# Kernel optimization log

Hardware: AMD Instinct MI355X
Metric: run time of the kernel (lower is better)

The kernel has to match this reference:

```python
import jax, jax.numpy as jnp
import numpy as np

L = 4        # num decoder layers
H = 8        # heads
D = 512      # d_model
DFF = 2048   # ffn hidden
V = 8000     # target vocab
B = 16       # batch
S_ENC = 128  # encoder seq len
T = 32       # decode target_length
START, END, NULL = 1, 2, 0
NEG = -1e9
EPS = 1e-6


def sinusoid_pos(max_len, d):
    pos = np.arange(max_len)[:, None].astype(np.float32)
    i = np.arange(d)[None, :].astype(np.float32)
    ang = pos / np.power(10000.0, (2.0 * np.floor(i / 2.0)) / d)
    pe = np.where(np.arange(d)[None, :] % 2 == 0, np.sin(ang), np.cos(ang))
    return jnp.asarray(pe[None], jnp.float32)  # [1, max_len, d]


def setup_inputs() -> dict:
    key = jax.random.key(0)
    ks = jax.random.split(key, 16)
    g = lambda k, shape: jax.random.normal(k, shape, jnp.float32) * 0.02
    return {
        "target_length": T,
        "encoder_output": jax.random.normal(ks[0], (B, S_ENC, D), jnp.float32),
        "padding_mask": jnp.zeros((B, S_ENC), jnp.float32),  # 1.0 where padded
        "embed": g(ks[1], (V, D)),
        "wq": g(ks[2], (L, D, D)), "wk": g(ks[3], (L, D, D)),
        "wv": g(ks[4], (L, D, D)), "wo": g(ks[5], (L, D, D)),
        "cwq": g(ks[6], (L, D, D)), "cwk": g(ks[7], (L, D, D)),
        "cwv": g(ks[8], (L, D, D)), "cwo": g(ks[9], (L, D, D)),
        "w1": g(ks[10], (L, D, DFF)), "b1": jnp.zeros((L, DFF), jnp.float32),
        "w2": g(ks[11], (L, DFF, D)), "b2": jnp.zeros((L, D), jnp.float32),
        "ln_g": jnp.ones((L, 3, D), jnp.float32), "ln_b": jnp.zeros((L, 3, D), jnp.float32),
        "fc_w": g(ks[12], (D, V)), "fc_b": jnp.zeros((V,), jnp.float32),
    }


def ln(x, g, b):
    m = jnp.mean(x, axis=-1, keepdims=True)
    v = jnp.mean(jnp.square(x - m), axis=-1, keepdims=True)
    return (x - m) * jax.lax.rsqrt(v + EPS) * g + b


def mha(q_in, kv_in, wq, wk, wv, wo, mask):
    Bn, Sq, d = q_in.shape
    dh = d // H
    q = (q_in @ wq).reshape(Bn, Sq, H, dh)
    k = (kv_in @ wk).reshape(Bn, -1, H, dh)
    v = (kv_in @ wv).reshape(Bn, -1, H, dh)
    s = jnp.einsum('bqhd,bkhd->bhqk', q, k) / jnp.sqrt(jnp.float32(dh)) + mask
    a = jax.nn.softmax(s, axis=-1)
    o = jnp.einsum('bhqk,bkhd->bqhd', a, v).reshape(Bn, Sq, d)
    return o @ wo


def decoder_stack(x, encoder_output, self_mask, cross_mask,
                  wq, wk, wv, wo, cwq, cwk, cwv, cwo,
                  w1, b1, w2, b2, ln_g, ln_b):
    for i in range(L):
        a = mha(x, x, wq[i], wk[i], wv[i], wo[i], self_mask)
        x = ln(x + a, ln_g[i, 0], ln_b[i, 0])
        a2 = mha(x, encoder_output, cwq[i], cwk[i], cwv[i], cwo[i], cross_mask)
        x = ln(x + a2, ln_g[i, 1], ln_b[i, 1])
        f = jax.nn.relu(x @ w1[i] + b1[i]) @ w2[i] + b2[i]
        x = ln(x + f, ln_g[i, 2], ln_b[i, 2])
    return x


def reference(target_length, encoder_output, padding_mask, embed,
              wq, wk, wv, wo, cwq, cwk, cwv, cwo,
              w1, b1, w2, b2, ln_g, ln_b, fc_w, fc_b):
    Bn, S, d = encoder_output.shape
    Tp1 = target_length + 1
    pos_enc = sinusoid_pos(Tp1, d)
    sqrt_d = jnp.sqrt(jnp.float32(d))
    cross_mask = padding_mask[:, None, None, :] * NEG  # [B,1,1,S_enc]
    tokens0 = jnp.full((Bn, Tp1), NULL, jnp.int32).at[:, 0].set(START)
    done0 = jnp.zeros((Bn,), bool)

    def step(carry, t):
        tokens, done = carry
        # re-embed the whole (fixed-size, masked) prefix buffer each step
        x = embed[tokens] * sqrt_d + pos_enc
        # only positions <= t are valid keys; no look-ahead mask (matches original)
        self_mask = jnp.where(jnp.arange(Tp1) <= t, 0.0, NEG)[None, None, None, :]
        x = decoder_stack(x, encoder_output, self_mask, cross_mask,
                          wq, wk, wv, wo, cwq, cwk, cwv, cwo,
                          w1, b1, w2, b2, ln_g, ln_b)
        out = x[:, t, :] @ fc_w + fc_b  # logits at last valid position
        max_idx = jnp.argmax(out, axis=-1).astype(jnp.int32)
        done = done | (max_idx == END)
        tok = jnp.where(done, jnp.int32(NULL), max_idx)
        tokens = tokens.at[:, t + 1].set(tok)
        return (tokens, done), None

    (tokens, done), _ = jax.lax.scan(step, (tokens0, done0), jnp.arange(target_length))
    return tokens[:, 1:].astype(jnp.int64)
```

## Files before the change

kernel.cpp:

```cpp
#include <hip/hip_runtime.h>
#include <math.h>

#define L_   4
#define H_   8
#define D_   512
#define DH   64
#define DFF_ 2048
#define V_   8000
#define B_   16
#define SENC 128
#define T_   32
#define TP1  33
#define NEGV -1e9f
#define EPSV 1e-6f
#define SQRTD 22.627416997969522f
#define XSZ  ((size_t)TP1 * B_ * D_)

__global__ __launch_bounds__(128) void gemm32_k(
    const float* __restrict__ A, const float* __restrict__ W,
    const float* __restrict__ bias, float* __restrict__ C,
    int M, int N, int K, int kchunk, size_t pstride, int relu, int tmode)
{
    __shared__ __align__(16) float As[16][32];
    __shared__ __align__(16) float Bs[16][64];
    int tid = threadIdx.x;
    int tx = tid & 15, ty = tid >> 4;
    int m0 = blockIdx.y * 32, n0 = blockIdx.x * 64;
    int kbeg = blockIdx.z * kchunk, kend = kbeg + kchunk;
    C += (size_t)blockIdx.z * pstride;
    int am = tid >> 2, aseg = tid & 3;
    int bk = tid >> 4, bc4 = (tid & 15) * 4;
    float acc[4][4] = {};
    for (int k0 = kbeg; k0 < kend; k0 += 16) {
        int gm = m0 + am;
        float4 av = make_float4(0.f, 0.f, 0.f, 0.f);
        if (gm < M) av = *(const float4*)&A[(size_t)gm * K + k0 + aseg * 4];
        As[aseg * 4 + 0][am] = av.x;
        As[aseg * 4 + 1][am] = av.y;
        As[aseg * 4 + 2][am] = av.z;
        As[aseg * 4 + 3][am] = av.w;
        *(float4*)&Bs[bk][bc4] =
            *(const float4*)&W[(size_t)(k0 + bk) * N + n0 + bc4];
        *(float4*)&Bs[bk + 8][bc4] =
            *(const float4*)&W[(size_t)(k0 + bk + 8) * N + n0 + bc4];
        __syncthreads();
        #pragma unroll
        for (int kk = 0; kk < 16; kk++) {
            float4 a4 = *(const float4*)&As[kk][ty * 4];
            float4 b4 = *(const float4*)&Bs[kk][tx * 4];
            float a[4] = {a4.x, a4.y, a4.z, a4.w};
            float b[4] = {b4.x, b4.y, b4.z, b4.w};
            #pragma unroll
            for (int i = 0; i < 4; i++)
                #pragma unroll
                for (int j = 0; j < 4; j++)
                    acc[i][j] += a[i] * b[j];
        }
        __syncthreads();
    }
    #pragma unroll
    for (int i = 0; i < 4; i++) {
        int gm = m0 + ty * 4 + i;
        if (gm >= M) continue;
        #pragma unroll
        for (int j = 0; j < 4; j++) {
            int gn = n0 + tx * 4 + j;
            float v = acc[i][j];
            if (bias) v += bias[gn];
            if (relu) v = fmaxf(v, 0.f);
            if (tmode == 1)
                C[(size_t)(gm >> 7) * 65536 + (size_t)gn * SENC + (gm & 127)] = v;
            else
                C[(size_t)gm * N + gn] = v;
        }
    }
}

__global__ __launch_bounds__(128) void gemm_qkv_k(
    const float* __restrict__ A, const float* __restrict__ W0,
    const float* __restrict__ W1, const float* __restrict__ W2,
    float* __restrict__ Cb, int M)
{
    __shared__ __align__(16) float As[16][32];
    __shared__ __align__(16) float Bs[16][64];
    int sel = blockIdx.x >> 3;
    const float* W = (sel == 0) ? W0 : ((sel == 1) ? W1 : W2);
    float* C = Cb + (size_t)sel * XSZ;
    int tid = threadIdx.x;
    int tx = tid & 15, ty = tid >> 4;
    int m0 = blockIdx.y * 32, n0 = (blockIdx.x & 7) * 64;
    int am = tid >> 2, aseg = tid & 3;
    int bk = tid >> 4, bc4 = (tid & 15) * 4;
    float acc[4][4] = {};
    for (int k0 = 0; k0 < D_; k0 += 16) {
        int gm = m0 + am;
        float4 av = make_float4(0.f, 0.f, 0.f, 0.f);
        if (gm < M) av = *(const float4*)&A[(size_t)gm * D_ + k0 + aseg * 4];
        As[aseg * 4 + 0][am] = av.x;
        As[aseg * 4 + 1][am] = av.y;
        As[aseg * 4 + 2][am] = av.z;
        As[aseg * 4 + 3][am] = av.w;
        *(float4*)&Bs[bk][bc4] =
            *(const float4*)&W[(size_t)(k0 + bk) * D_ + n0 + bc4];
        *(float4*)&Bs[bk + 8][bc4] =
            *(const float4*)&W[(size_t)(k0 + bk + 8) * D_ + n0 + bc4];
        __syncthreads();
        #pragma unroll
        for (int kk = 0; kk < 16; kk++) {
            float4 a4 = *(const float4*)&As[kk][ty * 4];
            float4 b4 = *(const float4*)&Bs[kk][tx * 4];
            float a[4] = {a4.x, a4.y, a4.z, a4.w};
            float b[4] = {b4.x, b4.y, b4.z, b4.w};
            #pragma unroll
            for (int i = 0; i < 4; i++)
                #pragma unroll
                for (int j = 0; j < 4; j++)
                    acc[i][j] += a[i] * b[j];
        }
        __syncthreads();
    }
    #pragma unroll
    for (int i = 0; i < 4; i++) {
        int gm = m0 + ty * 4 + i;
        if (gm >= M) continue;
        #pragma unroll
        for (int j = 0; j < 4; j++) {
            int gn = n0 + tx * 4 + j;
            if (sel == 1)
                C[(size_t)(gm & 15) * 16896 + (size_t)gn * TP1 + (gm >> 4)] =
                    acc[i][j];
            else
                C[(size_t)gm * D_ + gn] = acc[i][j];
        }
    }
}

__global__ void init_k(int* __restrict__ tokens, int* __restrict__ done,
                       float* __restrict__ cmask, const float* __restrict__ pm)
{
    int tid = threadIdx.x + blockIdx.x * 256;
    if (tid < B_ * TP1) tokens[tid] = ((tid % TP1) == 0) ? 1 : 0;
    if (tid < B_) done[tid] = 0;
    if (tid < B_ * SENC) cmask[tid] = pm[tid] * NEGV;
}

__global__ __launch_bounds__(256) void embed_k(
    const float* __restrict__ embed, const int* __restrict__ tokens,
    float* __restrict__ x)
{
    int p = blockIdx.x;
    int b = blockIdx.y;
    int tok = tokens[b * TP1 + p];
    const float* e = embed + (size_t)tok * D_;
    float* xr = x + ((size_t)p * B_ + b) * D_;
    for (int d = threadIdx.x; d < D_; d += 256) {
        float fd = (float)(2 * (d / 2)) / (float)D_;
        float ang = (float)p / powf(10000.f, fd);
        float pe = (d & 1) ? cosf(ang) : sinf(ang);
        xr[d] = e[d] * SQRTD + pe;
    }
}

__device__ __forceinline__ float block_sum(float s) {
    __shared__ float red[4];
    #pragma unroll
    for (int off = 32; off; off >>= 1) s += __shfl_xor(s, off);
    if ((threadIdx.x & 63) == 0) red[threadIdx.x >> 6] = s;
    __syncthreads();
    float tot = red[0] + red[1] + red[2] + red[3];
    __syncthreads();
    return tot;
}

__global__ __launch_bounds__(256) void self_fused_k(
    const float* __restrict__ q, const float* __restrict__ kT,
    const float* __restrict__ v, const float* __restrict__ wo,
    float* __restrict__ x, const float* __restrict__ gam,
    const float* __restrict__ bet, int P)
{
    int r = blockIdx.x;
    int b = r & 15;
    int tid = threadIdx.x;
    __shared__ float qrow[D_], attnrow[D_];
    __shared__ float scs[H_][32];
    __shared__ float inv[H_];
    qrow[tid]       = q[(size_t)r * D_ + tid];
    qrow[tid + 256] = q[(size_t)r * D_ + tid + 256];
    __syncthreads();
    {
        int kp = tid & 31, h = tid >> 5;
        float acc = 0.f;
        if (kp < P) {
            const float* kb = kT + ((size_t)(b * 8 + h) * 64) * TP1 + kp;
            for (int d = 0; d < 64; d++)
                acc += qrow[h * 64 + d] * kb[(size_t)d * TP1];
        }
        scs[h][kp] = acc * 0.125f;
    }
    __syncthreads();
    if (tid < 8) {
        float mx = -1e30f;
        for (int j = 0; j < P; j++) mx = fmaxf(mx, scs[tid][j]);
        float sum = 0.f;
        for (int j = 0; j < P; j++) {
            float e = expf(scs[tid][j] - mx);
            scs[tid][j] = e;
            sum += e;
        }
        inv[tid] = 1.f / sum;
    }
    __syncthreads();
    {
        int h0 = tid >> 6, h1 = h0 + 4;
        float o0 = 0.f, o1 = 0.f;
        for (int j = 0; j < P; j++) {
            const float* vr = v + ((size_t)j * B_ + b) * D_;
            o0 += scs[h0][j] * vr[tid];
            o1 += scs[h1][j] * vr[tid + 256];
        }
        attnrow[tid]       = o0 * inv[h0];
        attnrow[tid + 256] = o1 * inv[h1];
    }
    __syncthreads();
    float v0 = x[(size_t)r * D_ + tid];
    float v1 = x[(size_t)r * D_ + tid + 256];
    for (int k0 = 0; k0 < D_; k0++) {
        float a = attnrow[k0];
        v0 += a * wo[(size_t)k0 * D_ + tid];
        v1 += a * wo[(size_t)k0 * D_ + tid + 256];
    }
    float mean = block_sum(v0 + v1) * (1.f / 512.f);
    float d0 = v0 - mean, d1 = v1 - mean;
    float var = block_sum(d0 * d0 + d1 * d1) * (1.f / 512.f);
    float rs = rsqrtf(var + EPSV);
    x[(size_t)r * D_ + tid]       = d0 * rs * gam[tid] + bet[tid];
    x[(size_t)r * D_ + tid + 256] = d1 * rs * gam[tid + 256] + bet[tid + 256];
}

__global__ __launch_bounds__(256) void cross_fused_k(
    const float* __restrict__ KcT, const float* __restrict__ Vc,
    const float* __restrict__ cmask, const float* __restrict__ cwq,
    const float* __restrict__ cwo, float* __restrict__ x,
    const float* __restrict__ gam, const float* __restrict__ bet)
{
    int r = blockIdx.x;
    int b = r & 15;
    int tid = threadIdx.x;
    __shared__ float xs[D_], qrow[D_], attnrow[D_];
    __shared__ float scs[H_][SENC];
    __shared__ float inv[H_];
    xs[tid]       = x[(size_t)r * D_ + tid];
    xs[tid + 256] = x[(size_t)r * D_ + tid + 256];
    __syncthreads();
    {
        float q0 = 0.f, q1 = 0.f;
        for (int k0 = 0; k0 < D_; k0++) {
            float a = xs[k0];
            q0 += a * cwq[(size_t)k0 * D_ + tid];
            q1 += a * cwq[(size_t)k0 * D_ + tid + 256];
        }
        qrow[tid] = q0;
        qrow[tid + 256] = q1;
    }
    __syncthreads();
    #pragma unroll
    for (int j = 0; j < 4; j++) {
        int idx = tid + j * 256;
        int h = idx >> 7, s = idx & 127;
        const float* kb = KcT + ((size_t)(b * 512 + h * 64)) * SENC + s;
        float acc = 0.f;
        for (int d = 0; d < 64; d++)
            acc += qrow[h * 64 + d] * kb[(size_t)d * SENC];
        scs[h][s] = acc * 0.125f + cmask[b * SENC + s];
    }
    __syncthreads();
    if (tid < 8) {
        float mx = -1e30f;
        for (int s = 0; s < SENC; s++) mx = fmaxf(mx, scs[tid][s]);
        float sum = 0.f;
        for (int s = 0; s < SENC; s++) {
            float e = expf(scs[tid][s] - mx);
            scs[tid][s] = e;
            sum += e;
        }
        inv[tid] = 1.f / sum;
    }
    __syncthreads();
    {
        int h0 = tid >> 6, h1 = h0 + 4;
        float o0 = 0.f, o1 = 0.f;
        for (int s = 0; s < SENC; s++) {
            const float* vr = Vc + ((size_t)b * SENC + s) * D_;
            o0 += scs[h0][s] * vr[tid];
            o1 += scs[h1][s] * vr[tid + 256];
        }
        attnrow[tid]       = o0 * inv[h0];
        attnrow[tid + 256] = o1 * inv[h1];
    }
    __syncthreads();
    float v0 = xs[tid];
    float v1 = xs[tid + 256];
    for (int k0 = 0; k0 < D_; k0++) {
        float a = attnrow[k0];
        v0 += a * cwo[(size_t)k0 * D_ + tid];
        v1 += a * cwo[(size_t)k0 * D_ + tid + 256];
    }
    float mean = block_sum(v0 + v1) * (1.f / 512.f);
    float d0 = v0 - mean, d1 = v1 - mean;
    float var = block_sum(d0 * d0 + d1 * d1) * (1.f / 512.f);
    float rs = rsqrtf(var + EPSV);
    x[(size_t)r * D_ + tid]       = d0 * rs * gam[tid] + bet[tid];
    x[(size_t)r * D_ + tid + 256] = d1 * rs * gam[tid + 256] + bet[tid + 256];
}

__global__ __launch_bounds__(256) void ln_red_k(
    float* __restrict__ x, const float* __restrict__ parts, size_t pstride,
    int nparts, const float* __restrict__ bias,
    const float* __restrict__ gam, const float* __restrict__ bet)
{
    int r = blockIdx.x;
    float* xr = x + (size_t)r * D_;
    int tid = threadIdx.x;
    float v0 = xr[tid];
    float v1 = xr[tid + 256];
    for (int s = 0; s < nparts; s++) {
        const float* pr = parts + (size_t)s * pstride + (size_t)r * D_;
        v0 += pr[tid];
        v1 += pr[tid + 256];
    }
    if (bias) { v0 += bias[tid]; v1 += bias[tid + 256]; }
    float mean = block_sum(v0 + v1) * (1.f / 512.f);
    float d0 = v0 - mean, d1 = v1 - mean;
    float var = block_sum(d0 * d0 + d1 * d1) * (1.f / 512.f);
    float rs = rsqrtf(var + EPSV);
    xr[tid]       = d0 * rs * gam[tid] + bet[tid];
    xr[tid + 256] = d1 * rs * gam[tid + 256] + bet[tid + 256];
}

__global__ __launch_bounds__(256) void logits_k(
    const float* __restrict__ x, const float* __restrict__ fcw,
    const float* __restrict__ fcb, float* __restrict__ logits, int t)
{
    __shared__ float xs[B_][D_];
    __shared__ float red[4][64][B_];
    int tid = threadIdx.x;
    for (int i = tid; i < B_ * D_; i += 256) {
        int b = i >> 9, d = i & 511;
        xs[b][d] = x[((size_t)t * B_ + b) * D_ + d];
    }
    __syncthreads();
    int lane = tid & 63, ks = tid >> 6;
    int col = blockIdx.x * 64 + lane;
    float acc[B_] = {};
    int kb = ks * 128;
    for (int k = kb; k < kb + 128; k++) {
        float w = fcw[(size_t)k * V_ + col];
        #pragma unroll
        for (int b = 0; b < B_; b++) acc[b] += xs[b][k] * w;
    }
    #pragma unroll
    for (int b = 0; b < B_; b++) red[ks][lane][b] = acc[b];
    __syncthreads();
    if (ks == 0) {
        float bias = fcb[col];
        #pragma unroll
        for (int b = 0; b < B_; b++) {
            float s = red[0][lane][b] + red[1][lane][b]
                    + red[2][lane][b] + red[3][lane][b];
            logits[(size_t)b * V_ + col] = s + bias;
        }
    }
}

__global__ __launch_bounds__(256) void argmax_k(
    const float* __restrict__ logits, int* __restrict__ tokens,
    int* __restrict__ done, int t)
{
    int b = blockIdx.x;
    const float* lr = logits + (size_t)b * V_;
    float bv = -1e30f; int bi = 0x7fffffff;
    for (int v = threadIdx.x; v < V_; v += 256) {
        float val = lr[v];
        if (val > bv) { bv = val; bi = v; }
    }
    __shared__ float sv[256];
    __shared__ int si[256];
    sv[threadIdx.x] = bv; si[threadIdx.x] = bi;
    __syncthreads();
    for (int s = 128; s; s >>= 1) {
        if (threadIdx.x < s) {
            float ov = sv[threadIdx.x + s]; int oi = si[threadIdx.x + s];
            if (ov > sv[threadIdx.x] ||
                (ov == sv[threadIdx.x] && oi < si[threadIdx.x])) {
                sv[threadIdx.x] = ov; si[threadIdx.x] = oi;
            }
        }
        __syncthreads();
    }
    if (threadIdx.x == 0) {
        int idx = si[0];
        int dn = done[b] | (idx == 2 ? 1 : 0);
        done[b] = dn;
        tokens[b * TP1 + t + 1] = dn ? 0 : idx;
    }
}

__global__ void writeout_k(const int* __restrict__ tokens, int* __restrict__ out)
{
    int i = threadIdx.x + blockIdx.x * 256;
    if (i < B_ * T_) {
        int b = i / T_, j = i % T_;
        out[i] = tokens[b * TP1 + j + 1];
    }
}

extern "C" void kernel_launch(void* const* d_in, const int* in_sizes, int n_in,
                              void* d_out, int out_size, void* d_ws, size_t ws_size,
                              hipStream_t stream)
{
    const float* enc   = (const float*)d_in[1];
    const float* pm    = (const float*)d_in[2];
    const float* embed = (const float*)d_in[3];
    const float* wq    = (const float*)d_in[4];
    const float* wk    = (const float*)d_in[5];
    const float* wv    = (const float*)d_in[6];
    const float* wo    = (const float*)d_in[7];
    const float* cwq   = (const float*)d_in[8];
    const float* cwk   = (const float*)d_in[9];
    const float* cwv   = (const float*)d_in[10];
    const float* cwo   = (const float*)d_in[11];
    const float* w1    = (const float*)d_in[12];
    const float* b1    = (const float*)d_in[13];
    const float* w2    = (const float*)d_in[14];
    const float* b2    = (const float*)d_in[15];
    const float* ln_g  = (const float*)d_in[16];
    const float* ln_b  = (const float*)d_in[17];
    const float* fcw   = (const float*)d_in[18];
    const float* fcb   = (const float*)d_in[19];

    float* ws = (float*)d_ws;
    size_t off = 0;
    float* x     = ws + off; off += XSZ;
    float* qkv   = ws + off; off += 3 * XSZ;
    float* parts = ws + off; off += 4 * XSZ;
    float* ffnh  = ws + off; off += (size_t)TP1 * B_ * DFF_;
    float* logits= ws + off; off += (size_t)B_ * V_;
    float* KcT   = ws + off; off += (size_t)L_ * B_ * SENC * D_;
    float* Vc    = ws + off; off += (size_t)L_ * B_ * SENC * D_;
    float* cmask = ws + off; off += (size_t)B_ * SENC;
    int* tokens  = (int*)(ws + off); off += (B_ * TP1 + 63) & ~63;
    int* done    = (int*)(ws + off); off += 64;

    init_k<<<8, 256, 0, stream>>>(tokens, done, cmask, pm);

    const size_t KVL = (size_t)B_ * SENC * D_;
    for (int l = 0; l < L_; l++) {
        gemm32_k<<<dim3(8, (B_ * SENC) / 32), 128, 0, stream>>>(
            enc, cwk + (size_t)l * D_ * D_, nullptr, KcT + l * KVL,
            B_ * SENC, D_, D_, D_, 0, 0, 1);
        gemm32_k<<<dim3(8, (B_ * SENC) / 32), 128, 0, stream>>>(
            enc, cwv + (size_t)l * D_ * D_, nullptr, Vc + l * KVL,
            B_ * SENC, D_, D_, D_, 0, 0, 0);
    }

    for (int t = 0; t < T_; t++) {
        int P = t + 1;
        int M = P * B_;
        int mt = (M + 31) / 32;

        embed_k<<<dim3(P, B_), 256, 0, stream>>>(embed, tokens, x);

        for (int l = 0; l < L_; l++) {
            const size_t lw = (size_t)l * D_ * D_;
            gemm_qkv_k<<<dim3(24, mt), 128, 0, stream>>>(
                x, wq + lw, wk + lw, wv + lw, qkv, M);
            self_fused_k<<<M, 256, 0, stream>>>(
                qkv, qkv + XSZ, qkv + 2 * XSZ, wo + lw, x,
                ln_g + (size_t)(l * 3 + 0) * D_, ln_b + (size_t)(l * 3 + 0) * D_, P);
            cross_fused_k<<<M, 256, 0, stream>>>(
                KcT + l * KVL, Vc + l * KVL, cmask, cwq + lw, cwo + lw, x,
                ln_g + (size_t)(l * 3 + 1) * D_, ln_b + (size_t)(l * 3 + 1) * D_);
            gemm32_k<<<dim3(32, mt), 128, 0, stream>>>(
                x, w1 + (size_t)l * D_ * DFF_, b1 + (size_t)l * DFF_, ffnh,
                M, DFF_, D_, D_, 0, 1, 0);
            gemm32_k<<<dim3(8, mt, 4), 128, 0, stream>>>(
                ffnh, w2 + (size_t)l * DFF_ * D_, nullptr, parts,
                M, D_, DFF_, 512, XSZ, 0, 0);
            ln_red_k<<<M, 256, 0, stream>>>(x, parts, XSZ, 4, b2 + (size_t)l * D_,
                ln_g + (size_t)(l * 3 + 2) * D_, ln_b + (size_t)(l * 3 + 2) * D_);
        }

        logits_k<<<V_ / 64, 256, 0, stream>>>(x, fcw, fcb, logits, t);
        argmax_k<<<B_, 256, 0, stream>>>(logits, tokens, done, t);
    }

    writeout_k<<<2, 256, 0, stream>>>(tokens, (int*)d_out);
}
```

Measured before the change: 27.11 ms.

## Double-buffer GEMM tiles, fuse self and cross attention, fold argmax into logits

The GEMM kernels move to 256 threads with 2x4 micro-tiles, padded double-buffered shared tiles and register prefetch of the next k-slice, aiming to overlap loads with compute. The self-attention and cross-attention fused kernels become one kernel per row, removing a launch and a round trip of x through global memory. The logits kernel now does a per-block argmax and writes 125 candidates per batch row, so the final argmax reads candidates instead of full logits. Costs include smaller per-thread work in the GEMM, which may lower ILP, and a longer serial mega kernel per row.

```diff
diff --git a/kernel.cpp b/kernel.cpp
--- a/kernel.cpp
+++ b/kernel.cpp
@@ -16,73 +16,96 @@
 #define SQRTD 22.627416997969522f
 #define XSZ  ((size_t)TP1 * B_ * D_)
 
-__global__ __launch_bounds__(128) void gemm32_k(
+__global__ __launch_bounds__(256) void gemm32_k(
     const float* __restrict__ A, const float* __restrict__ W,
     const float* __restrict__ bias, float* __restrict__ C,
     int M, int N, int K, int kchunk, size_t pstride, int relu, int tmode)
 {
-    __shared__ __align__(16) float As[16][32];
-    __shared__ __align__(16) float Bs[16][64];
+    __shared__ __align__(16) float As[2][16][34];
+    __shared__ __align__(16) float Bs[2][16][68];
     int tid = threadIdx.x;
     int tx = tid & 15, ty = tid >> 4;
     int m0 = blockIdx.y * 32, n0 = blockIdx.x * 64;
-    int kbeg = blockIdx.z * kchunk, kend = kbeg + kchunk;
+    int kbeg = blockIdx.z * kchunk;
+    int niter = kchunk >> 4;
     C += (size_t)blockIdx.z * pstride;
     int am = tid >> 2, aseg = tid & 3;
     int bk = tid >> 4, bc4 = (tid & 15) * 4;
-    float acc[4][4] = {};
-    for (int k0 = kbeg; k0 < kend; k0 += 16) {
-        int gm = m0 + am;
-        float4 av = make_float4(0.f, 0.f, 0.f, 0.f);
-        if (gm < M) av = *(const float4*)&A[(size_t)gm * K + k0 + aseg * 4];
-        As[aseg * 4 + 0][am] = av.x;
-        As[aseg * 4 + 1][am] = av.y;
-        As[aseg * 4 + 2][am] = av.z;
-        As[aseg * 4 + 3][am] = av.w;
-        *(float4*)&Bs[bk][bc4] =
-            *(const float4*)&W[(size_t)(k0 + bk) * N + n0 + bc4];
-        *(float4*)&Bs[bk + 8][bc4] =
-            *(const float4*)&W[(size_t)(k0 + bk + 8) * N + n0 + bc4];
-        __syncthreads();
+    float4 aReg = make_float4(0.f, 0.f, 0.f, 0.f), bReg;
+    {
+        int k0 = kbeg;
+        if (tid < 128) {
+            int gm = m0 + am;
+            if (gm < M) aReg = *(const float4*)&A[(size_t)gm * K + k0 + aseg * 4];
+        }
+        bReg = *(const float4*)&W[(size_t)(k0 + bk) * N + n0 + bc4];
+    }
+    if (tid < 128) {
+        As[0][aseg * 4 + 0][am] = aReg.x;
+        As[0][aseg * 4 + 1][am] = aReg.y;
+        As[0][aseg * 4 + 2][am] = aReg.z;
+        As[0][aseg * 4 + 3][am] = aReg.w;
+    }
+    *(float4*)&Bs[0][bk][bc4] = bReg;
+    __syncthreads();
+    float acc[2][4] = {};
+    for (int it = 0; it < niter; it++) {
+        int cur = it & 1;
+        if (it + 1 < niter) {
+            int k0 = kbeg + (it + 1) * 16;
+            if (tid < 128) {
+                int gm = m0 + am;
+                aReg = make_float4(0.f, 0.f, 0.f, 0.f);
+                if (gm < M) aReg = *(const float4*)&A[(size_t)gm * K + k0 + aseg * 4];
+            }
+            bReg = *(const float4*)&W[(size_t)(k0 + bk) * N + n0 + bc4];
+        }
         #pragma unroll
         for (int kk = 0; kk < 16; kk++) {
-            float4 a4 = *(const float4*)&As[kk][ty * 4];
-            float4 b4 = *(const float4*)&Bs[kk][tx * 4];
-            float a[4] = {a4.x, a4.y, a4.z, a4.w};
-            float b[4] = {b4.x, b4.y, b4.z, b4.w};
-            #pragma unroll
-            for (int i = 0; i < 4; i++)
-                #pragma unroll
-                for (int j = 0; j < 4; j++)
-                    acc[i][j] += a[i] * b[j];
+            float2 a2 = *(const float2*)&As[cur][kk][ty * 2];
+            float4 b4 = *(const float4*)&Bs[cur][kk][tx * 4];
+            acc[0][0] += a2.x * b4.x; acc[0][1] += a2.x * b4.y;
+            acc[0][2] += a2.x * b4.z; acc[0][3] += a2.x * b4.w;
+            acc[1][0] += a2.y * b4.x; acc[1][1] += a2.y * b4.y;
+            acc[1][2] += a2.y * b4.z; acc[1][3] += a2.y * b4.w;
+        }
+        if (it + 1 < niter) {
+            int nxt = 1 - cur;
+            if (tid < 128) {
+                As[nxt][aseg * 4 + 0][am] = aReg.x;
+                As[nxt][aseg * 4 + 1][am] = aReg.y;
+                As[nxt][aseg * 4 + 2][am] = aReg.z;
+                As[nxt][aseg * 4 + 3][am] = aReg.w;
+            }
+            *(float4*)&Bs[nxt][bk][bc4] = bReg;
         }
         __syncthreads();
     }
     #pragma unroll
-    for (int i = 0; i < 4; i++) {
-        int gm = m0 + ty * 4 + i;
+    for (int i = 0; i < 2; i++) {
+        int gm = m0 + ty * 2 + i;
         if (gm >= M) continue;
         #pragma unroll
         for (int j = 0; j < 4; j++) {
             int gn = n0 + tx * 4 + j;
-            float v = acc[i][j];
-            if (bias) v += bias[gn];
-            if (relu) v = fmaxf(v, 0.f);
+            float vv = acc[i][j];
+            if (bias) vv += bias[gn];
+            if (relu) vv = fmaxf(vv, 0.f);
             if (tmode == 1)
-                C[(size_t)(gm >> 7) * 65536 + (size_t)gn * SENC + (gm & 127)] = v;
+                C[(size_t)(gm >> 7) * 65536 + (size_t)gn * SENC + (gm & 127)] = vv;
             else
-                C[(size_t)gm * N + gn] = v;
-        }
-    }
-}
-
-__global__ __launch_bounds__(128) void gemm_qkv_k(
+                C[(size_t)gm * N + gn] = vv;
+        }
+    }
+}
+
+__global__ __launch_bounds__(256) void gemm_qkv_k(
     const float* __restrict__ A, const float* __restrict__ W0,
     const float* __restrict__ W1, const float* __restrict__ W2,
     float* __restrict__ Cb, int M)
 {
-    __shared__ __align__(16) float As[16][32];
-    __shared__ __align__(16) float Bs[16][64];
+    __shared__ __align__(16) float As[2][16][34];
+    __shared__ __align__(16) float Bs[2][16][68];
     int sel = blockIdx.x >> 3;
     const float* W = (sel == 0) ? W0 : ((sel == 1) ? W1 : W2);
     float* C = Cb + (size_t)sel * XSZ;
@@ -91,37 +114,58 @@
     int m0 = blockIdx.y * 32, n0 = (blockIdx.x & 7) * 64;
     int am = tid >> 2, aseg = tid & 3;
     int bk = tid >> 4, bc4 = (tid & 15) * 4;
-    float acc[4][4] = {};
-    for (int k0 = 0; k0 < D_; k0 += 16) {
-        int gm = m0 + am;
-        float4 av = make_float4(0.f, 0.f, 0.f, 0.f);
-        if (gm < M) av = *(const float4*)&A[(size_t)gm * D_ + k0 + aseg * 4];
-        As[aseg * 4 + 0][am] = av.x;
-        As[aseg * 4 + 1][am] = av.y;
-        As[aseg * 4 + 2][am] = av.z;
-        As[aseg * 4 + 3][am] = av.w;
-        *(float4*)&Bs[bk][bc4] =
-            *(const float4*)&W[(size_t)(k0 + bk) * D_ + n0 + bc4];
-        *(float4*)&Bs[bk + 8][bc4] =
-            *(const float4*)&W[(size_t)(k0 + bk + 8) * D_ + n0 + bc4];
-        __syncthreads();
+    float4 aReg = make_float4(0.f, 0.f, 0.f, 0.f), bReg;
+    {
+        if (tid < 128) {
+            int gm = m0 + am;
+            if (gm < M) aReg = *(const float4*)&A[(size_t)gm * D_ + aseg * 4];
+        }
+        bReg = *(const float4*)&W[(size_t)bk * D_ + n0 + bc4];
+    }
+    if (tid < 128) {
+        As[0][aseg * 4 + 0][am] = aReg.x;
+        As[0][aseg * 4 + 1][am] = aReg.y;
+        As[0][aseg * 4 + 2][am] = aReg.z;
+        As[0][aseg * 4 + 3][am] = aReg.w;
+    }
+    *(float4*)&Bs[0][bk][bc4] = bReg;
+    __syncthreads();
+    float acc[2][4] = {};
+    for (int it = 0; it < 32; it++) {
+        int cur = it & 1;
+        if (it + 1 < 32) {
+            int k0 = (it + 1) * 16;
+            if (tid < 128) {
+                int gm = m0 + am;
+                aReg = make_float4(0.f, 0.f, 0.f, 0.f);
+                if (gm < M) aReg = *(const float4*)&A[(size_t)gm * D_ + k0 + aseg * 4];
+            }
+            bReg = *(const float4*)&W[(size_t)(k0 + bk) * D_ + n0 + bc4];
+        }
         #pragma unroll
         for (int kk = 0; kk < 16; kk++) {
-            float4 a4 = *(const float4*)&As[kk][ty * 4];
-            float4 b4 = *(const float4*)&Bs[kk][tx * 4];
-            float a[4] = {a4.x, a4.y, a4.z, a4.w};
-            float b[4] = {b4.x, b4.y, b4.z, b4.w};
-            #pragma unroll
-            for (int i = 0; i < 4; i++)
-                #pragma unroll
-                for (int j = 0; j < 4; j++)
-                    acc[i][j] += a[i] * b[j];
+            float2 a2 = *(const float2*)&As[cur][kk][ty * 2];
+            float4 b4 = *(const float4*)&Bs[cur][kk][tx * 4];
+            acc[0][0] += a2.x * b4.x; acc[0][1] += a2.x * b4.y;
+            acc[0][2] += a2.x * b4.z; acc[0][3] += a2.x * b4.w;
+            acc[1][0] += a2.y * b4.x; acc[1][1] += a2.y * b4.y;
+            acc[1][2] += a2.y * b4.z; acc[1][3] += a2.y * b4.w;
+        }
+        if (it + 1 < 32) {
+            int nxt = 1 - cur;
+            if (tid < 128) {
+                As[nxt][aseg * 4 + 0][am] = aReg.x;
+                As[nxt][aseg * 4 + 1][am] = aReg.y;
+                As[nxt][aseg * 4 + 2][am] = aReg.z;
+                As[nxt][aseg * 4 + 3][am] = aReg.w;
+            }
+            *(float4*)&Bs[nxt][bk][bc4] = bReg;
         }
         __syncthreads();
     }
     #pragma unroll
-    for (int i = 0; i < 4; i++) {
-        int gm = m0 + ty * 4 + i;
+    for (int i = 0; i < 2; i++) {
+        int gm = m0 + ty * 2 + i;
         if (gm >= M) continue;
         #pragma unroll
         for (int j = 0; j < 4; j++) {
@@ -172,28 +216,28 @@
     return tot;
 }
 
-__global__ __launch_bounds__(256) void self_fused_k(
+__global__ __launch_bounds__(256) void attn_mega_k(
     const float* __restrict__ q, const float* __restrict__ kT,
     const float* __restrict__ v, const float* __restrict__ wo,
-    float* __restrict__ x, const float* __restrict__ gam,
-    const float* __restrict__ bet, int P)
-{
-    int r = blockIdx.x;
-    int b = r & 15;
+    const float* __restrict__ KcT, const float* __restrict__ Vc,
+    const float* __restrict__ cmask, const float* __restrict__ cwq,
+    const float* __restrict__ cwo, float* __restrict__ x,
+    const float* __restrict__ lg, const float* __restrict__ lb, int P)
+{
+    int r = blockIdx.x, b = r & 15;
     int tid = threadIdx.x;
-    __shared__ float qrow[D_], attnrow[D_];
-    __shared__ float scs[H_][32];
+    int c0 = tid * 2;
+    __shared__ float xs[D_], arow[D_];
+    __shared__ float scs[H_][SENC];
     __shared__ float inv[H_];
-    qrow[tid]       = q[(size_t)r * D_ + tid];
-    qrow[tid + 256] = q[(size_t)r * D_ + tid + 256];
-    __syncthreads();
     {
         int kp = tid & 31, h = tid >> 5;
         float acc = 0.f;
         if (kp < P) {
+            const float* qr = q + (size_t)r * D_ + h * 64;
             const float* kb = kT + ((size_t)(b * 8 + h) * 64) * TP1 + kp;
-            for (int d = 0; d < 64; d++)
-                acc += qrow[h * 64 + d] * kb[(size_t)d * TP1];
+            #pragma unroll 8
+            for (int d = 0; d < 64; d++) acc += qr[d] * kb[(size_t)d * TP1];
         }
         scs[h][kp] = acc * 0.125f;
     }
@@ -211,56 +255,43 @@
     }
     __syncthreads();
     {
-        int h0 = tid >> 6, h1 = h0 + 4;
+        int h = c0 >> 6;
         float o0 = 0.f, o1 = 0.f;
         for (int j = 0; j < P; j++) {
-            const float* vr = v + ((size_t)j * B_ + b) * D_;
-            o0 += scs[h0][j] * vr[tid];
-            o1 += scs[h1][j] * vr[tid + 256];
-        }
-        attnrow[tid]       = o0 * inv[h0];
-        attnrow[tid + 256] = o1 * inv[h1];
-    }
-    __syncthreads();
-    float v0 = x[(size_t)r * D_ + tid];
-    float v1 = x[(size_t)r * D_ + tid + 256];
-    for (int k0 = 0; k0 < D_; k0++) {
-        float a = attnrow[k0];
-        v0 += a * wo[(size_t)k0 * D_ + tid];
-        v1 += a * wo[(size_t)k0 * D_ + tid + 256];
-    }
-    float mean = block_sum(v0 + v1) * (1.f / 512.f);
-    float d0 = v0 - mean, d1 = v1 - mean;
-    float var = block_sum(d0 * d0 + d1 * d1) * (1.f / 512.f);
-    float rs = rsqrtf(var + EPSV);
-    x[(size_t)r * D_ + tid]       = d0 * rs * gam[tid] + bet[tid];
-    x[(size_t)r * D_ + tid + 256] = d1 * rs * gam[tid + 256] + bet[tid + 256];
-}
-
-__global__ __launch_bounds__(256) void cross_fused_k(
-    const float* __restrict__ KcT, const float* __restrict__ Vc,
-    const float* __restrict__ cmask, const float* __restrict__ cwq,
-    const float* __restrict__ cwo, float* __restrict__ x,
-    const float* __restrict__ gam, const float* __restrict__ bet)
-{
-    int r = blockIdx.x;
-    int b = r & 15;
-    int tid = threadIdx.x;
-    __shared__ float xs[D_], qrow[D_], attnrow[D_];
-    __shared__ float scs[H_][SENC];
-    __shared__ float inv[H_];
-    xs[tid]       = x[(size_t)r * D_ + tid];
-    xs[tid + 256] = x[(size_t)r * D_ + tid + 256];
+            float2 vv = *(const float2*)&v[((size_t)j * B_ + b) * D_ + c0];
+            float w = scs[h][j];
+            o0 += w * vv.x; o1 += w * vv.y;
+        }
+        arow[c0]     = o0 * inv[h];
+        arow[c0 + 1] = o1 * inv[h];
+    }
+    __syncthreads();
+    {
+        float2 xv = *(const float2*)&x[(size_t)r * D_ + c0];
+        float v0 = xv.x, v1 = xv.y;
+        #pragma unroll 8
+        for (int k = 0; k < D_; k++) {
+            float a = arow[k];
+            float2 wv = *(const float2*)&wo[(size_t)k * D_ + c0];
+            v0 += a * wv.x; v1 += a * wv.y;
+        }
+        float mean = block_sum(v0 + v1) * (1.f / 512.f);
+        float d0 = v0 - mean, d1 = v1 - mean;
+        float var = block_sum(d0 * d0 + d1 * d1) * (1.f / 512.f);
+        float rs = rsqrtf(var + EPSV);
+        xs[c0]     = d0 * rs * lg[c0]     + lb[c0];
+        xs[c0 + 1] = d1 * rs * lg[c0 + 1] + lb[c0 + 1];
+    }
     __syncthreads();
     {
         float q0 = 0.f, q1 = 0.f;
-        for (int k0 = 0; k0 < D_; k0++) {
-            float a = xs[k0];
-            q0 += a * cwq[(size_t)k0 * D_ + tid];
-            q1 += a * cwq[(size_t)k0 * D_ + tid + 256];
-        }
-        qrow[tid] = q0;
-        qrow[tid + 256] = q1;
+        #pragma unroll 8
+        for (int k = 0; k < D_; k++) {
+            float a = xs[k];
+            float2 wv = *(const float2*)&cwq[(size_t)k * D_ + c0];
+            q0 += a * wv.x; q1 += a * wv.y;
+        }
+        arow[c0] = q0; arow[c0 + 1] = q1;
     }
     __syncthreads();
     #pragma unroll
@@ -269,8 +300,8 @@
         int h = idx >> 7, s = idx & 127;
         const float* kb = KcT + ((size_t)(b * 512 + h * 64)) * SENC + s;
         float acc = 0.f;
-        for (int d = 0; d < 64; d++)
-            acc += qrow[h * 64 + d] * kb[(size_t)d * SENC];
+        #pragma unroll 8
+        for (int d = 0; d < 64; d++) acc += arow[h * 64 + d] * kb[(size_t)d * SENC];
         scs[h][s] = acc * 0.125f + cmask[b * SENC + s];
     }
     __syncthreads();
@@ -287,30 +318,32 @@
     }
     __syncthreads();
     {
-        int h0 = tid >> 6, h1 = h0 + 4;
+        int h = c0 >> 6;
         float o0 = 0.f, o1 = 0.f;
         for (int s = 0; s < SENC; s++) {
-            const float* vr = Vc + ((size_t)b * SENC + s) * D_;
-            o0 += scs[h0][s] * vr[tid];
-            o1 += scs[h1][s] * vr[tid + 256];
-        }
-        attnrow[tid]       = o0 * inv[h0];
-        attnrow[tid + 256] = o1 * inv[h1];
-    }
-    __syncthreads();
-    float v0 = xs[tid];
-    float v1 = xs[tid + 256];
-    for (int k0 = 0; k0 < D_; k0++) {
-        float a = attnrow[k0];
-        v0 += a * cwo[(size_t)k0 * D_ + tid];
-        v1 += a * cwo[(size_t)k0 * D_ + tid + 256];
-    }
-    float mean = block_sum(v0 + v1) * (1.f / 512.f);
-    float d0 = v0 - mean, d1 = v1 - mean;
-    float var = block_sum(d0 * d0 + d1 * d1) * (1.f / 512.f);
-    float rs = rsqrtf(var + EPSV);
-    x[(size_t)r * D_ + tid]       = d0 * rs * gam[tid] + bet[tid];
-    x[(size_t)r * D_ + tid + 256] = d1 * rs * gam[tid + 256] + bet[tid + 256];
+            float2 vv = *(const float2*)&Vc[((size_t)b * SENC + s) * D_ + c0];
+            float w = scs[h][s];
+            o0 += w * vv.x; o1 += w * vv.y;
+        }
+        arow[c0]     = o0 * inv[h];
+        arow[c0 + 1] = o1 * inv[h];
+    }
+    __syncthreads();
+    {
+        float v0 = xs[c0], v1 = xs[c0 + 1];
+        #pragma unroll 8
+        for (int k = 0; k < D_; k++) {
+            float a = arow[k];
+            float2 wv = *(const float2*)&cwo[(size_t)k * D_ + c0];
+            v0 += a * wv.x; v1 += a * wv.y;
+        }
+        float mean = block_sum(v0 + v1) * (1.f / 512.f);
+        float d0 = v0 - mean, d1 = v1 - mean;
+        float var = block_sum(d0 * d0 + d1 * d1) * (1.f / 512.f);
+        float rs = rsqrtf(var + EPSV);
+        x[(size_t)r * D_ + c0]     = d0 * rs * lg[D_ + c0]     + lb[D_ + c0];
+        x[(size_t)r * D_ + c0 + 1] = d1 * rs * lg[D_ + c0 + 1] + lb[D_ + c0 + 1];
+    }
 }
 
 __global__ __launch_bounds__(256) void ln_red_k(
@@ -339,7 +372,8 @@
 
 __global__ __launch_bounds__(256) void logits_k(
     const float* __restrict__ x, const float* __restrict__ fcw,
-    const float* __restrict__ fcb, float* __restrict__ logits, int t)
+    const float* __restrict__ fcb, float* __restrict__ cand_v,
+    int* __restrict__ cand_i, int t)
 {
     __shared__ float xs[B_][D_];
     __shared__ float red[4][64][B_];
@@ -365,43 +399,49 @@
         float bias = fcb[col];
         #pragma unroll
         for (int b = 0; b < B_; b++) {
-            float s = red[0][lane][b] + red[1][lane][b]
-                    + red[2][lane][b] + red[3][lane][b];
-            logits[(size_t)b * V_ + col] = s + bias;
-        }
-    }
-}
-
-__global__ __launch_bounds__(256) void argmax_k(
-    const float* __restrict__ logits, int* __restrict__ tokens,
-    int* __restrict__ done, int t)
+            float val = red[0][lane][b] + red[1][lane][b]
+                      + red[2][lane][b] + red[3][lane][b] + bias;
+            int idx = col;
+            #pragma unroll
+            for (int off = 32; off; off >>= 1) {
+                float ov = __shfl_down(val, off);
+                int oi = __shfl_down(idx, off);
+                if (ov > val || (ov == val && oi < idx)) { val = ov; idx = oi; }
+            }
+            if (lane == 0) {
+                cand_v[(size_t)b * 125 + blockIdx.x] = val;
+                cand_i[(size_t)b * 125 + blockIdx.x] = idx;
+            }
+        }
+    }
+}
+
+__global__ __launch_bounds__(128) void argmax_k(
+    const float* __restrict__ cand_v, const int* __restrict__ cand_i,
+    int* __restrict__ tokens, int* __restrict__ done, int t)
 {
     int b = blockIdx.x;
-    const float* lr = logits + (size_t)b * V_;
-    float bv = -1e30f; int bi = 0x7fffffff;
-    for (int v = threadIdx.x; v < V_; v += 256) {
-        float val = lr[v];
-        if (val > bv) { bv = val; bi = v; }
-    }
-    __shared__ float sv[256];
-    __shared__ int si[256];
-    sv[threadIdx.x] = bv; si[threadIdx.x] = bi;
-    __syncthreads();
-    for (int s = 128; s; s >>= 1) {
-        if (threadIdx.x < s) {
-            float ov = sv[threadIdx.x + s]; int oi = si[threadIdx.x + s];
-            if (ov > sv[threadIdx.x] ||
-                (ov == sv[threadIdx.x] && oi < si[threadIdx.x])) {
-                sv[threadIdx.x] = ov; si[threadIdx.x] = oi;
+    int tid = threadIdx.x;
+    float val = -1e30f; int idx = 0x7fffffff;
+    if (tid < 125) { val = cand_v[(size_t)b * 125 + tid]; idx = cand_i[(size_t)b * 125 + tid]; }
+    __shared__ float sv[128];
+    __shared__ int si[128];
+    sv[tid] = val; si[tid] = idx;
+    __syncthreads();
+    for (int s = 64; s; s >>= 1) {
+        if (tid < s) {
+            float ov = sv[tid + s]; int oi = si[tid + s];
+            if (ov > sv[tid] || (ov == sv[tid] && oi < si[tid])) {
+                sv[tid] = ov; si[tid] = oi;
             }
         }
         __syncthreads();
     }
-    if (threadIdx.x == 0) {
-        int idx = si[0];
-        int dn = done[b] | (idx == 2 ? 1 : 0);
+    if (tid == 0) {
+        int best = si[0];
+        int dn = done[b] | (best == 2 ? 1 : 0);
         done[b] = dn;
-        tokens[b * TP1 + t + 1] = dn ? 0 : idx;
+        tokens[b * TP1 + t + 1] = dn ? 0 : best;
     }
 }
 
@@ -444,10 +484,11 @@
     float* qkv   = ws + off; off += 3 * XSZ;
     float* parts = ws + off; off += 4 * XSZ;
     float* ffnh  = ws + off; off += (size_t)TP1 * B_ * DFF_;
-    float* logits= ws + off; off += (size_t)B_ * V_;
+    float* cand_v= ws + off; off += (size_t)B_ * 125;
     float* KcT   = ws + off; off += (size_t)L_ * B_ * SENC * D_;
     float* Vc    = ws + off; off += (size_t)L_ * B_ * SENC * D_;
     float* cmask = ws + off; off += (size_t)B_ * SENC;
+    int* cand_i  = (int*)(ws + off); off += (size_t)B_ * 125;
     int* tokens  = (int*)(ws + off); off += (B_ * TP1 + 63) & ~63;
     int* done    = (int*)(ws + off); off += 64;
 
@@ -455,10 +496,10 @@
 
     const size_t KVL = (size_t)B_ * SENC * D_;
     for (int l = 0; l < L_; l++) {
-        gemm32_k<<<dim3(8, (B_ * SENC) / 32), 128, 0, stream>>>(
+        gemm32_k<<<dim3(8, (B_ * SENC) / 32), 256, 0, stream>>>(
             enc, cwk + (size_t)l * D_ * D_, nullptr, KcT + l * KVL,
             B_ * SENC, D_, D_, D_, 0, 0, 1);
-        gemm32_k<<<dim3(8, (B_ * SENC) / 32), 128, 0, stream>>>(
+        gemm32_k<<<dim3(8, (B_ * SENC) / 32), 256, 0, stream>>>(
             enc, cwv + (size_t)l * D_ * D_, nullptr, Vc + l * KVL,
             B_ * SENC, D_, D_, D_, 0, 0, 0);
     }
@@ -472,26 +513,24 @@
 
         for (int l = 0; l < L_; l++) {
             const size_t lw = (size_t)l * D_ * D_;
-            gemm_qkv_k<<<dim3(24, mt), 128, 0, stream>>>(
+            gemm_qkv_k<<<dim3(24, mt), 256, 0, stream>>>(
                 x, wq + lw, wk + lw, wv + lw, qkv, M);
-            self_fused_k<<<M, 256, 0, stream>>>(
-                qkv, qkv + XSZ, qkv + 2 * XSZ, wo + lw, x,
+            attn_mega_k<<<M, 256, 0, stream>>>(
+                qkv, qkv + XSZ, qkv + 2 * XSZ, wo + lw,
+                KcT + l * KVL, Vc + l * KVL, cmask, cwq + lw, cwo + lw, x,
                 ln_g + (size_t)(l * 3 + 0) * D_, ln_b + (size_t)(l * 3 + 0) * D_, P);
-            cross_fused_k<<<M, 256, 0, stream>>>(
-                KcT + l * KVL, Vc + l * KVL, cmask, cwq + lw, cwo + lw, x,
-                ln_g + (size_t)(l * 3 + 1) * D_, ln_b + (size_t)(l * 3 + 1) * D_);
-            gemm32_k<<<dim3(32, mt), 128, 0, stream>>>(
+            gemm32_k<<<dim3(32, mt), 256, 0, stream>>>(
                 x, w1 + (size_t)l * D_ * DFF_, b1 + (size_t)l * DFF_, ffnh,
                 M, DFF_, D_, D_, 0, 1, 0);
-            gemm32_k<<<dim3(8, mt, 4), 128, 0, stream>>>(
+            gemm32_k<<<dim3(8, mt, 4), 256, 0, stream>>>(
                 ffnh, w2 + (size_t)l * DFF_ * D_, nullptr, parts,
                 M, D_, DFF_, 512, XSZ, 0, 0);
             ln_red_k<<<M, 256, 0, stream>>>(x, parts, XSZ, 4, b2 + (size_t)l * D_,
                 ln_g + (size_t)(l * 3 + 2) * D_, ln_b + (size_t)(l * 3 + 2) * D_);
         }
 
-        logits_k<<<V_ / 64, 256, 0, stream>>>(x, fcw, fcb, logits, t);
-        argmax_k<<<B_, 256, 0, stream>>>(logits, tokens, done, t);
+        logits_k<<<V_ / 64, 256, 0, stream>>>(x, fcw, fcb, cand_v, cand_i, t);
+        argmax_k<<<B_, 128, 0, stream>>>(cand_v, cand_i, tokens, done, t);
     }
 
     writeout_k<<<2, 256, 0, stream>>>(tokens, (int*)d_out);
```

Result: faster. 24.32 ms (-10.3%).
